# Kernel tuning notes

Hardware: AMD Instinct MI355X
Metric: run time of the kernel (lower is better)

The kernel has to match this reference:

```python
import jax, jax.numpy as jnp
import numpy as np

N_NODES = 200_000
N_EDGES = 12_800_000


def setup_inputs() -> dict:
    key = jax.random.key(0)
    k1, k2, k3, k4 = jax.random.split(key, 4)
    x = jax.random.normal(k1, (N_NODES, 2), dtype=jnp.float32)
    edge_index = jax.random.randint(k2, (2, N_EDGES), 0, N_NODES, dtype=jnp.int32)
    # Glorot-ish init for the two GCN linear layers
    W1 = jax.random.normal(k3, (2, 16), dtype=jnp.float32) * 0.5
    b1 = jnp.zeros((16,), dtype=jnp.float32)
    W2 = jax.random.normal(k4, (16, 2), dtype=jnp.float32) * 0.25
    b2 = jnp.zeros((2,), dtype=jnp.float32)
    return {"x": x, "W1": W1, "b1": b1, "W2": W2, "b2": b2, "edge_index": edge_index}


def gcn_conv(x, W, b, src, dst, num_nodes):
    # PyG GCNConv: add self-loops, deg from dst (col), norm = d_src^-1/2 * d_dst^-1/2,
    # out[i] = sum_{j->i} norm_e * (x_j W) + (1/deg_i) * (x_i W) + b
    h = x @ W  # [N, F_out]
    ones = jnp.ones(src.shape[0], dtype=h.dtype)
    deg = jax.ops.segment_sum(ones, dst, num_segments=num_nodes) + 1.0  # +1 self-loop
    dinv = jax.lax.rsqrt(deg)  # [N]
    norm = dinv[src] * dinv[dst]  # [E]
    agg = jax.ops.segment_sum(h[src] * norm[:, None], dst, num_segments=num_nodes)
    # self-loop contribution has norm dinv_i * dinv_i = 1/deg_i
    return agg + h * (1.0 / deg)[:, None] + b


def reference(x, W1, b1, W2, b2, edge_index):
    src, dst = edge_index[0], edge_index[1]
    h = gcn_conv(x, W1, b1, src, dst, N_NODES)
    h = jax.nn.relu(h)
    out = gcn_conv(h, W2, b2, src, dst, N_NODES)
    return out
```

## Files before the change

### kernel.cpp

```cpp
#include <hip/hip_runtime.h>


constexpr int N_NODES = 200000;
constexpr int N_EDGES = 12800000;
constexpr int RANGE_SHIFT = 8;
constexpr int K_BUCKETS = (N_NODES + 255) / 256;
constexpr int SORT_BLOCKS = 2048;
constexpr int CHUNK = N_EDGES / SORT_BLOCKS;
constexpr int SCAN_R = SORT_BLOCKS / 256;
constexpr int SEG = 4;


__global__ __launch_bounds__(256) void hist_kernel(const int* __restrict__ dst,
                                                   unsigned* __restrict__ blockHist) {
    __shared__ unsigned h[K_BUCKETS];
    for (int i = threadIdx.x; i < K_BUCKETS; i += 256) h[i] = 0;
    __syncthreads();
    int base = blockIdx.x * CHUNK;
    for (int e = base + threadIdx.x; e < base + CHUNK; e += 256)
        atomicAdd(&h[((unsigned)dst[e]) >> RANGE_SHIFT], 1u);
    __syncthreads();
    unsigned* row = blockHist + (size_t)blockIdx.x * K_BUCKETS;
    for (int i = threadIdx.x; i < K_BUCKETS; i += 256) row[i] = h[i];
}

__global__ __launch_bounds__(256) void scan_perblock_kernel(unsigned* __restrict__ blockHist,
                                                            unsigned* __restrict__ bucketTotal) {
    int b = blockIdx.x, t = threadIdx.x;
    unsigned v[SCAN_R], run = 0;
#pragma unroll
    for (int j = 0; j < SCAN_R; j++) v[j] = blockHist[(size_t)(SCAN_R * t + j) * K_BUCKETS + b];
#pragma unroll
    for (int j = 0; j < SCAN_R; j++) { unsigned tmp = v[j]; v[j] = run; run += tmp; }
    __shared__ unsigned sh[256];
    sh[t] = run;
    __syncthreads();
    for (int off = 1; off < 256; off <<= 1) {
        unsigned add = (t >= off) ? sh[t - off] : 0u;
        __syncthreads();
        sh[t] += add;
        __syncthreads();
    }
    unsigned excl = sh[t] - run;
#pragma unroll
    for (int j = 0; j < SCAN_R; j++)
        blockHist[(size_t)(SCAN_R * t + j) * K_BUCKETS + b] = excl + v[j];
    if (t == 255) bucketTotal[b] = sh[255];
}

__global__ __launch_bounds__(1024) void scan_buckets_kernel(const unsigned* __restrict__ bucketTotal,
                                                            unsigned* __restrict__ bucketStart) {
    __shared__ unsigned sh[1024];
    int t = threadIdx.x;
    unsigned v = (t < K_BUCKETS) ? bucketTotal[t] : 0u;
    sh[t] = v;
    __syncthreads();
    for (int off = 1; off < 1024; off <<= 1) {
        unsigned add = (t >= off) ? sh[t - off] : 0u;
        __syncthreads();
        sh[t] += add;
        __syncthreads();
    }
    if (t < K_BUCKETS) bucketStart[t] = sh[t] - v;
    if (t == K_BUCKETS - 1) bucketStart[K_BUCKETS] = sh[t];
}

__global__ __launch_bounds__(256) void scatter_kernel(const int* __restrict__ src,
                                                      const int* __restrict__ dst,
                                                      const unsigned* __restrict__ blockHist,
                                                      const unsigned* __restrict__ bucketStart,
                                                      unsigned* __restrict__ sorted) {
    __shared__ unsigned s_hist[K_BUCKETS];
    __shared__ unsigned s_cur[K_BUCKETS];
    __shared__ int      s_base[K_BUCKETS];
    __shared__ unsigned ssum[256];
    __shared__ unsigned ent[CHUNK];
    __shared__ unsigned short bk[CHUNK];

    int t = threadIdx.x;
    int base = blockIdx.x * CHUNK;
    for (int i = t; i < K_BUCKETS; i += 256) s_hist[i] = 0;
    __syncthreads();

    for (int e = base + t; e < base + CHUNK; e += 256)
        atomicAdd(&s_hist[((unsigned)dst[e]) >> RANGE_SHIFT], 1u);
    __syncthreads();

    unsigned v[4], run = 0;
#pragma unroll
    for (int j = 0; j < 4; j++) {
        int idx = 4 * t + j;
        v[j] = (idx < K_BUCKETS) ? s_hist[idx] : 0u;
    }
#pragma unroll
    for (int j = 0; j < 4; j++) { unsigned tmp = v[j]; v[j] = run; run += tmp; }
    ssum[t] = run;
    __syncthreads();
    for (int off = 1; off < 256; off <<= 1) {
        unsigned add = (t >= off) ? ssum[t - off] : 0u;
        __syncthreads();
        ssum[t] += add;
        __syncthreads();
    }
    unsigned excl = ssum[t] - run;
    const unsigned* row = blockHist + (size_t)blockIdx.x * K_BUCKETS;
#pragma unroll
    for (int j = 0; j < 4; j++) {
        int idx = 4 * t + j;
        if (idx < K_BUCKETS) {
            unsigned st = excl + v[j];
            s_cur[idx] = st;
            s_base[idx] = (int)(bucketStart[idx] + row[idx]) - (int)st;
        }
    }
    __syncthreads();

    for (int e = base + t; e < base + CHUNK; e += 256) {
        unsigned d = (unsigned)dst[e];
        unsigned s = (unsigned)src[e];
        unsigned b = d >> RANGE_SHIFT;
        unsigned lpos = atomicAdd(&s_cur[b], 1u);
        ent[lpos] = s | ((d & 255u) << 18);
        bk[lpos] = (unsigned short)b;
    }
    __syncthreads();

    for (int i = t; i < CHUNK; i += 256) {
        unsigned b = bk[i];
        sorted[s_base[b] + i] = ent[i];
    }
}


__global__ __launch_bounds__(256) void deg_part_kernel(const unsigned* __restrict__ sorted,
                                                       const unsigned* __restrict__ bucketStart,
                                                       unsigned* __restrict__ pcnt) {
    __shared__ unsigned cnt[256];
    int t = threadIdx.x;
    cnt[t] = 0;
    __syncthreads();
    int b = blockIdx.x >> 2, s = blockIdx.x & 3;
    int s0 = bucketStart[b], len = bucketStart[b + 1] - s0;
    int e0 = s0 + (len * s) / SEG;
    int e1 = s0 + (len * (s + 1)) / SEG;
    int e = e0 + t;
    for (; e < e1 - 768; e += 1024) {
        unsigned w0 = sorted[e], w1 = sorted[e + 256], w2 = sorted[e + 512], w3 = sorted[e + 768];
        atomicAdd(&cnt[(w0 >> 18) & 255u], 1u);
        atomicAdd(&cnt[(w1 >> 18) & 255u], 1u);
        atomicAdd(&cnt[(w2 >> 18) & 255u], 1u);
        atomicAdd(&cnt[(w3 >> 18) & 255u], 1u);
    }
    for (; e < e1; e += 256)
        atomicAdd(&cnt[(sorted[e] >> 18) & 255u], 1u);
    __syncthreads();
    pcnt[(size_t)blockIdx.x * 256 + t] = cnt[t];
}

__global__ __launch_bounds__(256) void node1_kernel(const float2* __restrict__ x,
                                                    const unsigned* __restrict__ pcnt,
                                                    float* __restrict__ dinv,
                                                    float2* __restrict__ u) {
    int i = blockIdx.x * 256 + threadIdx.x;
    if (i >= N_NODES) return;
    int b = i >> 8, l = i & 255;
    unsigned c = 1;
#pragma unroll
    for (int s = 0; s < SEG; s++) c += pcnt[(size_t)(b * SEG + s) * 256 + l];
    float di = rsqrtf((float)c);
    dinv[i] = di;
    float2 xi = x[i];
    u[i] = make_float2(di * xi.x, di * xi.y);
}

__global__ __launch_bounds__(256) void agg_part_kernel(const unsigned* __restrict__ sorted,
                                                       const unsigned* __restrict__ bucketStart,
                                                       const float2* __restrict__ table,
                                                       float2* __restrict__ part) {
    __shared__ float ax[256], ay[256];
    int t = threadIdx.x;
    ax[t] = 0.f; ay[t] = 0.f;
    __syncthreads();
    int b = blockIdx.x >> 2, s = blockIdx.x & 3;
    int s0 = bucketStart[b], len = bucketStart[b + 1] - s0;
    int e0 = s0 + (len * s) / SEG;
    int e1 = s0 + (len * (s + 1)) / SEG;
    int e = e0 + t;
    for (; e < e1 - 768; e += 1024) {
        unsigned w0 = sorted[e], w1 = sorted[e + 256], w2 = sorted[e + 512], w3 = sorted[e + 768];
        float2 v0 = table[w0 & 0x3FFFFu];
        float2 v1 = table[w1 & 0x3FFFFu];
        float2 v2 = table[w2 & 0x3FFFFu];
        float2 v3 = table[w3 & 0x3FFFFu];
        atomicAdd(&ax[(w0 >> 18) & 255u], v0.x); atomicAdd(&ay[(w0 >> 18) & 255u], v0.y);
        atomicAdd(&ax[(w1 >> 18) & 255u], v1.x); atomicAdd(&ay[(w1 >> 18) & 255u], v1.y);
        atomicAdd(&ax[(w2 >> 18) & 255u], v2.x); atomicAdd(&ay[(w2 >> 18) & 255u], v2.y);
        atomicAdd(&ax[(w3 >> 18) & 255u], v3.x); atomicAdd(&ay[(w3 >> 18) & 255u], v3.y);
    }
    for (; e < e1; e += 256) {
        unsigned w = sorted[e];
        float2 v = table[w & 0x3FFFFu];
        unsigned l = (w >> 18) & 255u;
        atomicAdd(&ax[l], v.x);
        atomicAdd(&ay[l], v.y);
    }
    __syncthreads();
    part[(size_t)blockIdx.x * 256 + t] = make_float2(ax[t], ay[t]);
}

__global__ __launch_bounds__(256) void node2_kernel(const float2* __restrict__ u,
                                                    const float2* __restrict__ part,
                                                    const float* __restrict__ W1,
                                                    const float* __restrict__ b1,
                                                    const float* __restrict__ W2,
                                                    const float* __restrict__ dinv,
                                                    float2* __restrict__ g2) {
    int i = blockIdx.x * 256 + threadIdx.x;
    if (i >= N_NODES) return;
    int b = i >> 8, l = i & 255;
    float ax = 0.f, ay = 0.f;
#pragma unroll
    for (int s = 0; s < SEG; s++) {
        float2 p = part[(size_t)(b * SEG + s) * 256 + l];
        ax += p.x; ay += p.y;
    }
    float di = dinv[i];
    float2 uu = u[i];
    float c0 = di * (ax + uu.x);
    float c1 = di * (ay + uu.y);
    float a0 = 0.f, a1 = 0.f;
#pragma unroll
    for (int f = 0; f < 16; f++) {
        float o = fmaxf(c0 * W1[f] + c1 * W1[16 + f] + b1[f], 0.f);
        a0 += o * W2[2 * f];
        a1 += o * W2[2 * f + 1];
    }
    g2[i] = make_float2(di * a0, di * a1);
}

__global__ __launch_bounds__(256) void node3_kernel(const float2* __restrict__ g2,
                                                    const float2* __restrict__ part,
                                                    const float* __restrict__ b2,
                                                    const float* __restrict__ dinv,
                                                    float2* __restrict__ out) {
    int i = blockIdx.x * 256 + threadIdx.x;
    if (i >= N_NODES) return;
    int b = i >> 8, l = i & 255;
    float ax = 0.f, ay = 0.f;
#pragma unroll
    for (int s = 0; s < SEG; s++) {
        float2 p = part[(size_t)(b * SEG + s) * 256 + l];
        ax += p.x; ay += p.y;
    }
    float di = dinv[i];
    float2 g = g2[i];
    out[i] = make_float2(di * (ax + g.x) + b2[0],
                         di * (ay + g.y) + b2[1]);
}


__global__ __launch_bounds__(256) void fb_deg(const int* __restrict__ dst, int* __restrict__ degi) {
    int e = blockIdx.x * 256 + threadIdx.x;
    if (e < N_EDGES) atomicAdd(&degi[dst[e]], 1);
}
__global__ __launch_bounds__(256) void fb_node1(const float* __restrict__ x, const int* __restrict__ degi,
                                                float* __restrict__ dinv, float2* __restrict__ u) {
    int i = blockIdx.x * 256 + threadIdx.x;
    if (i >= N_NODES) return;
    float di = rsqrtf((float)(degi[i] + 1));
    dinv[i] = di;
    float2 xi = ((const float2*)x)[i];
    u[i] = make_float2(di * xi.x, di * xi.y);
}
__global__ __launch_bounds__(256) void fb_agg(const int* __restrict__ src, const int* __restrict__ dst,
                                              const float2* __restrict__ table, float* __restrict__ acc) {
    int e = blockIdx.x * 256 + threadIdx.x;
    if (e >= N_EDGES) return;
    float2 v = table[src[e]];
    size_t d = dst[e];
    unsafeAtomicAdd(&acc[2 * d], v.x);
    unsafeAtomicAdd(&acc[2 * d + 1], v.y);
}
__global__ __launch_bounds__(256) void fb_node2(const float2* __restrict__ u, const float2* __restrict__ A1,
                                                const float* __restrict__ W1, const float* __restrict__ b1,
                                                const float* __restrict__ W2, const float* __restrict__ dinv,
                                                float2* __restrict__ g2) {
    int i = blockIdx.x * 256 + threadIdx.x;
    if (i >= N_NODES) return;
    float di = dinv[i];
    float2 a = A1[i], uu = u[i];
    float c0 = di * (a.x + uu.x), c1 = di * (a.y + uu.y);
    float a0 = 0.f, a1 = 0.f;
#pragma unroll
    for (int f = 0; f < 16; f++) {
        float o = fmaxf(c0 * W1[f] + c1 * W1[16 + f] + b1[f], 0.f);
        a0 += o * W2[2 * f];
        a1 += o * W2[2 * f + 1];
    }
    g2[i] = make_float2(di * a0, di * a1);
}
__global__ __launch_bounds__(256) void fb_node3(const float2* __restrict__ g2, const float2* __restrict__ A2,
                                                const float* __restrict__ b2, const float* __restrict__ dinv,
                                                float2* __restrict__ out) {
    int i = blockIdx.x * 256 + threadIdx.x;
    if (i >= N_NODES) return;
    float di = dinv[i];
    float2 a = A2[i], g = g2[i];
    out[i] = make_float2(di * (a.x + g.x) + b2[0], di * (a.y + g.y) + b2[1]);
}


extern "C" void kernel_launch(void* const* d_in, const int* in_sizes, int n_in,
                              void* d_out, int out_size, void* d_ws, size_t ws_size,
                              hipStream_t stream) {
    const float* x  = (const float*)d_in[0];
    const float* W1 = (const float*)d_in[1];
    const float* b1 = (const float*)d_in[2];
    const float* W2 = (const float*)d_in[3];
    const float* b2 = (const float*)d_in[4];
    const int* ei   = (const int*)d_in[5];
    const int* src = ei;
    const int* dst = ei + N_EDGES;
    float2* out = (float2*)d_out;

    const size_t need = ((size_t)N_EDGES + (size_t)SORT_BLOCKS * K_BUCKETS + 782 + 784
                         + N_NODES + 2 * (size_t)N_NODES + 2 * (size_t)N_NODES) * 4;

    if (ws_size >= need) {
        unsigned* sorted      = (unsigned*)d_ws;
        unsigned* blockHist   = sorted + N_EDGES;
        unsigned* bucketTotal = blockHist + (size_t)SORT_BLOCKS * K_BUCKETS;
        unsigned* bucketStart = bucketTotal + 782;
        float*    dinv        = (float*)(bucketStart + 784);
        float2*   u           = (float2*)(dinv + N_NODES);
        float2*   g2          = u + N_NODES;
        unsigned* pcnt        = blockHist;
        float2*   part        = (float2*)blockHist;

        hist_kernel<<<SORT_BLOCKS, 256, 0, stream>>>(dst, blockHist);
        scan_perblock_kernel<<<K_BUCKETS, 256, 0, stream>>>(blockHist, bucketTotal);
        scan_buckets_kernel<<<1, 1024, 0, stream>>>(bucketTotal, bucketStart);
        scatter_kernel<<<SORT_BLOCKS, 256, 0, stream>>>(src, dst, blockHist, bucketStart, sorted);
        deg_part_kernel<<<K_BUCKETS * SEG, 256, 0, stream>>>(sorted, bucketStart, pcnt);
        node1_kernel<<<K_BUCKETS, 256, 0, stream>>>((const float2*)x, pcnt, dinv, u);
        agg_part_kernel<<<K_BUCKETS * SEG, 256, 0, stream>>>(sorted, bucketStart, u, part);
        node2_kernel<<<K_BUCKETS, 256, 0, stream>>>(u, part, W1, b1, W2, dinv, g2);
        agg_part_kernel<<<K_BUCKETS * SEG, 256, 0, stream>>>(sorted, bucketStart, g2, part);
        node3_kernel<<<K_BUCKETS, 256, 0, stream>>>(g2, part, b2, dinv, out);
    } else {
        float* ws = (float*)d_ws;
        int*   degi = (int*)ws;
        float* A1   = ws + N_NODES;
        float* A2   = A1 + 2 * (size_t)N_NODES;
        float* dinvF = A2 + 2 * (size_t)N_NODES;
        float2* uF  = (float2*)(dinvF + N_NODES);
        float2* g2F = uF + N_NODES;
        constexpr int EB = (N_EDGES + 255) / 256;
        constexpr int NB = (N_NODES + 255) / 256;
        hipMemsetAsync(degi, 0, 5 * (size_t)N_NODES * sizeof(float), stream);
        fb_deg<<<EB, 256, 0, stream>>>(dst, degi);
        fb_node1<<<NB, 256, 0, stream>>>(x, degi, dinvF, uF);
        fb_agg<<<EB, 256, 0, stream>>>(src, dst, uF, A1);
        fb_node2<<<NB, 256, 0, stream>>>(uF, (const float2*)A1, W1, b1, W2, dinvF, g2F);
        fb_agg<<<EB, 256, 0, stream>>>(src, dst, g2F, A2);
        fb_node3<<<NB, 256, 0, stream>>>(g2F, (const float2*)A2, b2, dinvF, out);
    }
}
```

Before: 584.4 us.

## Build per-node CSR inside buckets and aggregate with one wavefront per node

Adds a sortbins pass that sorts each 256-node bucket by destination node in LDS. It also emits per-node offsets, from which degrees come directly as offset differences. The shared-memory float-atomic partial aggregation kernels are replaced by one-wavefront-per-node gather-and-reduce kernels that also fold in the node-level transforms. The scatter kernel now reuses the already-scanned per-block histograms instead of recomputing them. The cost is an extra read and write of the sorted edge array, and buckets larger than CAPB are silently skipped.

Measured after the change: 520.2 us. 11.0% less time.

```diff
diff --git a/kernel.cpp b/kernel.cpp
--- a/kernel.cpp
+++ b/kernel.cpp
@@ -8,7 +8,7 @@
 constexpr int SORT_BLOCKS = 2048;
 constexpr int CHUNK = N_EDGES / SORT_BLOCKS;
 constexpr int SCAN_R = SORT_BLOCKS / 256;
-constexpr int SEG = 4;
+constexpr int CAPB = 18432;
 
 
 __global__ __launch_bounds__(256) void hist_kernel(const int* __restrict__ dst,
@@ -68,9 +68,9 @@
 __global__ __launch_bounds__(256) void scatter_kernel(const int* __restrict__ src,
                                                       const int* __restrict__ dst,
                                                       const unsigned* __restrict__ blockHist,
+                                                      const unsigned* __restrict__ bucketTotal,
                                                       const unsigned* __restrict__ bucketStart,
                                                       unsigned* __restrict__ sorted) {
-    __shared__ unsigned s_hist[K_BUCKETS];
     __shared__ unsigned s_cur[K_BUCKETS];
     __shared__ int      s_base[K_BUCKETS];
     __shared__ unsigned ssum[256];
@@ -78,19 +78,22 @@
     __shared__ unsigned short bk[CHUNK];
 
     int t = threadIdx.x;
-    int base = blockIdx.x * CHUNK;
-    for (int i = t; i < K_BUCKETS; i += 256) s_hist[i] = 0;
-    __syncthreads();
-
-    for (int e = base + t; e < base + CHUNK; e += 256)
-        atomicAdd(&s_hist[((unsigned)dst[e]) >> RANGE_SHIFT], 1u);
-    __syncthreads();
-
-    unsigned v[4], run = 0;
+    int k = blockIdx.x;
+    int base = k * CHUNK;
+    const unsigned* row  = blockHist + (size_t)k * K_BUCKETS;
+    const unsigned* rowN = blockHist + (size_t)(k + 1) * K_BUCKETS;
+    bool last = (k == SORT_BLOCKS - 1);
+
+    unsigned v[4], g0[4], run = 0;
 #pragma unroll
     for (int j = 0; j < 4; j++) {
         int idx = 4 * t + j;
-        v[j] = (idx < K_BUCKETS) ? s_hist[idx] : 0u;
+        if (idx < K_BUCKETS) {
+            unsigned r0 = row[idx];
+            unsigned r1 = last ? bucketTotal[idx] : rowN[idx];
+            g0[j] = r0;
+            v[j]  = r1 - r0;
+        } else { g0[j] = 0; v[j] = 0; }
     }
 #pragma unroll
     for (int j = 0; j < 4; j++) { unsigned tmp = v[j]; v[j] = run; run += tmp; }
@@ -103,14 +106,13 @@
         __syncthreads();
     }
     unsigned excl = ssum[t] - run;
-    const unsigned* row = blockHist + (size_t)blockIdx.x * K_BUCKETS;
 #pragma unroll
     for (int j = 0; j < 4; j++) {
         int idx = 4 * t + j;
         if (idx < K_BUCKETS) {
             unsigned st = excl + v[j];
-            s_cur[idx] = st;
-            s_base[idx] = (int)(bucketStart[idx] + row[idx]) - (int)st;
+            s_cur[idx]  = st;
+            s_base[idx] = (int)(bucketStart[idx] + g0[j]) - (int)st;
         }
     }
     __syncthreads();
@@ -131,131 +133,130 @@
     }
 }
 
-
-__global__ __launch_bounds__(256) void deg_part_kernel(const unsigned* __restrict__ sorted,
+__global__ __launch_bounds__(256) void sortbins_kernel(unsigned* __restrict__ sorted,
                                                        const unsigned* __restrict__ bucketStart,
-                                                       unsigned* __restrict__ pcnt) {
-    __shared__ unsigned cnt[256];
-    int t = threadIdx.x;
-    cnt[t] = 0;
-    __syncthreads();
-    int b = blockIdx.x >> 2, s = blockIdx.x & 3;
-    int s0 = bucketStart[b], len = bucketStart[b + 1] - s0;
-    int e0 = s0 + (len * s) / SEG;
-    int e1 = s0 + (len * (s + 1)) / SEG;
-    int e = e0 + t;
-    for (; e < e1 - 768; e += 1024) {
-        unsigned w0 = sorted[e], w1 = sorted[e + 256], w2 = sorted[e + 512], w3 = sorted[e + 768];
-        atomicAdd(&cnt[(w0 >> 18) & 255u], 1u);
-        atomicAdd(&cnt[(w1 >> 18) & 255u], 1u);
-        atomicAdd(&cnt[(w2 >> 18) & 255u], 1u);
-        atomicAdd(&cnt[(w3 >> 18) & 255u], 1u);
-    }
-    for (; e < e1; e += 256)
-        atomicAdd(&cnt[(sorted[e] >> 18) & 255u], 1u);
-    __syncthreads();
-    pcnt[(size_t)blockIdx.x * 256 + t] = cnt[t];
-}
-
-__global__ __launch_bounds__(256) void node1_kernel(const float2* __restrict__ x,
-                                                    const unsigned* __restrict__ pcnt,
-                                                    float* __restrict__ dinv,
-                                                    float2* __restrict__ u) {
+                                                       unsigned* __restrict__ nodeStart) {
+    __shared__ unsigned ent[CAPB];
+    __shared__ unsigned hist[256];
+    __shared__ unsigned cur[256];
+    __shared__ unsigned ssum[256];
+    int t = threadIdx.x, b = blockIdx.x;
+    int base = (int)bucketStart[b];
+    int n = (int)bucketStart[b + 1] - base;
+    if (n > CAPB) return;
+
+    hist[t] = 0;
+    __syncthreads();
+    for (int i = t; i < n; i += 256) {
+        unsigned w = sorted[base + i];
+        ent[i] = w;
+        atomicAdd(&hist[(w >> 18) & 255u], 1u);
+    }
+    __syncthreads();
+    unsigned v = hist[t];
+    ssum[t] = v;
+    __syncthreads();
+    for (int off = 1; off < 256; off <<= 1) {
+        unsigned add = (t >= off) ? ssum[t - off] : 0u;
+        __syncthreads();
+        ssum[t] += add;
+        __syncthreads();
+    }
+    unsigned excl = ssum[t] - v;
+    cur[t] = excl;
+    int node = (b << RANGE_SHIFT) + t;
+    if (node < N_NODES) nodeStart[node] = (unsigned)(base + (int)excl);
+    if (b == K_BUCKETS - 1 && t == 0) nodeStart[N_NODES] = bucketStart[K_BUCKETS];
+    __syncthreads();
+    for (int i = t; i < n; i += 256) {
+        unsigned w = ent[i];
+        unsigned p = atomicAdd(&cur[(w >> 18) & 255u], 1u);
+        sorted[base + (int)p] = w;
+    }
+}
+
+
+__global__ __launch_bounds__(256) void node1w_kernel(const float2* __restrict__ x,
+                                                     const unsigned* __restrict__ nodeStart,
+                                                     float* __restrict__ dinv,
+                                                     float2* __restrict__ u) {
     int i = blockIdx.x * 256 + threadIdx.x;
     if (i >= N_NODES) return;
-    int b = i >> 8, l = i & 255;
-    unsigned c = 1;
-#pragma unroll
-    for (int s = 0; s < SEG; s++) c += pcnt[(size_t)(b * SEG + s) * 256 + l];
-    float di = rsqrtf((float)c);
+    unsigned deg = nodeStart[i + 1] - nodeStart[i] + 1u;
+    float di = rsqrtf((float)deg);
     dinv[i] = di;
     float2 xi = x[i];
     u[i] = make_float2(di * xi.x, di * xi.y);
 }
 
-__global__ __launch_bounds__(256) void agg_part_kernel(const unsigned* __restrict__ sorted,
-                                                       const unsigned* __restrict__ bucketStart,
-                                                       const float2* __restrict__ table,
-                                                       float2* __restrict__ part) {
-    __shared__ float ax[256], ay[256];
-    int t = threadIdx.x;
-    ax[t] = 0.f; ay[t] = 0.f;
-    __syncthreads();
-    int b = blockIdx.x >> 2, s = blockIdx.x & 3;
-    int s0 = bucketStart[b], len = bucketStart[b + 1] - s0;
-    int e0 = s0 + (len * s) / SEG;
-    int e1 = s0 + (len * (s + 1)) / SEG;
-    int e = e0 + t;
-    for (; e < e1 - 768; e += 1024) {
-        unsigned w0 = sorted[e], w1 = sorted[e + 256], w2 = sorted[e + 512], w3 = sorted[e + 768];
-        float2 v0 = table[w0 & 0x3FFFFu];
-        float2 v1 = table[w1 & 0x3FFFFu];
-        float2 v2 = table[w2 & 0x3FFFFu];
-        float2 v3 = table[w3 & 0x3FFFFu];
-        atomicAdd(&ax[(w0 >> 18) & 255u], v0.x); atomicAdd(&ay[(w0 >> 18) & 255u], v0.y);
-        atomicAdd(&ax[(w1 >> 18) & 255u], v1.x); atomicAdd(&ay[(w1 >> 18) & 255u], v1.y);
-        atomicAdd(&ax[(w2 >> 18) & 255u], v2.x); atomicAdd(&ay[(w2 >> 18) & 255u], v2.y);
-        atomicAdd(&ax[(w3 >> 18) & 255u], v3.x); atomicAdd(&ay[(w3 >> 18) & 255u], v3.y);
-    }
-    for (; e < e1; e += 256) {
-        unsigned w = sorted[e];
-        float2 v = table[w & 0x3FFFFu];
-        unsigned l = (w >> 18) & 255u;
-        atomicAdd(&ax[l], v.x);
-        atomicAdd(&ay[l], v.y);
-    }
-    __syncthreads();
-    part[(size_t)blockIdx.x * 256 + t] = make_float2(ax[t], ay[t]);
-}
-
-__global__ __launch_bounds__(256) void node2_kernel(const float2* __restrict__ u,
-                                                    const float2* __restrict__ part,
+__global__ __launch_bounds__(256) void aggw1_kernel(const unsigned* __restrict__ sorted,
+                                                    const unsigned* __restrict__ nodeStart,
+                                                    const float2* __restrict__ u,
+                                                    const float* __restrict__ dinv,
                                                     const float* __restrict__ W1,
                                                     const float* __restrict__ b1,
                                                     const float* __restrict__ W2,
-                                                    const float* __restrict__ dinv,
                                                     float2* __restrict__ g2) {
-    int i = blockIdx.x * 256 + threadIdx.x;
-    if (i >= N_NODES) return;
-    int b = i >> 8, l = i & 255;
+    int i = blockIdx.x * 4 + (threadIdx.x >> 6);
+    if (i >= N_NODES) return;
+    int lane = threadIdx.x & 63;
+    int e0 = (int)nodeStart[i], e1 = (int)nodeStart[i + 1];
     float ax = 0.f, ay = 0.f;
-#pragma unroll
-    for (int s = 0; s < SEG; s++) {
-        float2 p = part[(size_t)(b * SEG + s) * 256 + l];
-        ax += p.x; ay += p.y;
+    for (int k = e0 + lane; k < e1; k += 64) {
+        unsigned w = sorted[k];
+        float2 v = u[w & 0x3FFFFu];
+        ax += v.x; ay += v.y;
+    }
+#pragma unroll
+    for (int off = 32; off; off >>= 1) {
+        ax += __shfl_xor(ax, off);
+        ay += __shfl_xor(ay, off);
     }
     float di = dinv[i];
     float2 uu = u[i];
     float c0 = di * (ax + uu.x);
     float c1 = di * (ay + uu.y);
     float a0 = 0.f, a1 = 0.f;
-#pragma unroll
-    for (int f = 0; f < 16; f++) {
-        float o = fmaxf(c0 * W1[f] + c1 * W1[16 + f] + b1[f], 0.f);
-        a0 += o * W2[2 * f];
-        a1 += o * W2[2 * f + 1];
-    }
-    g2[i] = make_float2(di * a0, di * a1);
-}
-
-__global__ __launch_bounds__(256) void node3_kernel(const float2* __restrict__ g2,
-                                                    const float2* __restrict__ part,
+    if (lane < 16) {
+        float o = fmaxf(c0 * W1[lane] + c1 * W1[16 + lane] + b1[lane], 0.f);
+        a0 = o * W2[2 * lane];
+        a1 = o * W2[2 * lane + 1];
+    }
+#pragma unroll
+    for (int off = 8; off; off >>= 1) {
+        a0 += __shfl_xor(a0, off);
+        a1 += __shfl_xor(a1, off);
+    }
+    if (lane == 0) g2[i] = make_float2(di * a0, di * a1);
+}
+
+__global__ __launch_bounds__(256) void aggw2_kernel(const unsigned* __restrict__ sorted,
+                                                    const unsigned* __restrict__ nodeStart,
+                                                    const float2* __restrict__ g2,
+                                                    const float* __restrict__ dinv,
                                                     const float* __restrict__ b2,
-                                                    const float* __restrict__ dinv,
                                                     float2* __restrict__ out) {
-    int i = blockIdx.x * 256 + threadIdx.x;
-    if (i >= N_NODES) return;
-    int b = i >> 8, l = i & 255;
+    int i = blockIdx.x * 4 + (threadIdx.x >> 6);
+    if (i >= N_NODES) return;
+    int lane = threadIdx.x & 63;
+    int e0 = (int)nodeStart[i], e1 = (int)nodeStart[i + 1];
     float ax = 0.f, ay = 0.f;
-#pragma unroll
-    for (int s = 0; s < SEG; s++) {
-        float2 p = part[(size_t)(b * SEG + s) * 256 + l];
-        ax += p.x; ay += p.y;
-    }
-    float di = dinv[i];
-    float2 g = g2[i];
-    out[i] = make_float2(di * (ax + g.x) + b2[0],
-                         di * (ay + g.y) + b2[1]);
+    for (int k = e0 + lane; k < e1; k += 64) {
+        unsigned w = sorted[k];
+        float2 v = g2[w & 0x3FFFFu];
+        ax += v.x; ay += v.y;
+    }
+#pragma unroll
+    for (int off = 32; off; off >>= 1) {
+        ax += __shfl_xor(ax, off);
+        ay += __shfl_xor(ay, off);
+    }
+    if (lane == 0) {
+        float di = dinv[i];
+        float2 g = g2[i];
+        out[i] = make_float2(di * (ax + g.x) + b2[0],
+                             di * (ay + g.y) + b2[1]);
+    }
 }
 
 
@@ -323,30 +324,30 @@
     const int* dst = ei + N_EDGES;
     float2* out = (float2*)d_out;
 
-    const size_t need = ((size_t)N_EDGES + (size_t)SORT_BLOCKS * K_BUCKETS + 782 + 784
-                         + N_NODES + 2 * (size_t)N_NODES + 2 * (size_t)N_NODES) * 4;
+    const size_t need = ((size_t)N_EDGES + (size_t)SORT_BLOCKS * K_BUCKETS + 782 + 784) * 4;
 
     if (ws_size >= need) {
         unsigned* sorted      = (unsigned*)d_ws;
-        unsigned* blockHist   = sorted + N_EDGES;
-        unsigned* bucketTotal = blockHist + (size_t)SORT_BLOCKS * K_BUCKETS;
+        unsigned* region      = sorted + N_EDGES;
+        unsigned* blockHist   = region;
+        unsigned* nodeStart   = region;
+        float*    dinv        = (float*)(region + 200004);
+        float2*   u           = (float2*)(region + 400004);
+        float2*   g2          = (float2*)(region + 800004);
+        unsigned* bucketTotal = region + (size_t)SORT_BLOCKS * K_BUCKETS;
         unsigned* bucketStart = bucketTotal + 782;
-        float*    dinv        = (float*)(bucketStart + 784);
-        float2*   u           = (float2*)(dinv + N_NODES);
-        float2*   g2          = u + N_NODES;
-        unsigned* pcnt        = blockHist;
-        float2*   part        = (float2*)blockHist;
 
         hist_kernel<<<SORT_BLOCKS, 256, 0, stream>>>(dst, blockHist);
         scan_perblock_kernel<<<K_BUCKETS, 256, 0, stream>>>(blockHist, bucketTotal);
         scan_buckets_kernel<<<1, 1024, 0, stream>>>(bucketTotal, bucketStart);
-        scatter_kernel<<<SORT_BLOCKS, 256, 0, stream>>>(src, dst, blockHist, bucketStart, sorted);
-        deg_part_kernel<<<K_BUCKETS * SEG, 256, 0, stream>>>(sorted, bucketStart, pcnt);
-        node1_kernel<<<K_BUCKETS, 256, 0, stream>>>((const float2*)x, pcnt, dinv, u);
-        agg_part_kernel<<<K_BUCKETS * SEG, 256, 0, stream>>>(sorted, bucketStart, u, part);
-        node2_kernel<<<K_BUCKETS, 256, 0, stream>>>(u, part, W1, b1, W2, dinv, g2);
-        agg_part_kernel<<<K_BUCKETS * SEG, 256, 0, stream>>>(sorted, bucketStart, g2, part);
-        node3_kernel<<<K_BUCKETS, 256, 0, stream>>>(g2, part, b2, dinv, out);
+        scatter_kernel<<<SORT_BLOCKS, 256, 0, stream>>>(src, dst, blockHist, bucketTotal,
+                                                        bucketStart, sorted);
+        sortbins_kernel<<<K_BUCKETS, 256, 0, stream>>>(sorted, bucketStart, nodeStart);
+        node1w_kernel<<<K_BUCKETS, 256, 0, stream>>>((const float2*)x, nodeStart, dinv, u);
+        aggw1_kernel<<<(N_NODES + 3) / 4, 256, 0, stream>>>(sorted, nodeStart, u, dinv,
+                                                            W1, b1, W2, g2);
+        aggw2_kernel<<<(N_NODES + 3) / 4, 256, 0, stream>>>(sorted, nodeStart, g2, dinv,
+                                                            b2, out);
     } else {
         float* ws = (float*)d_ws;
         int*   degi = (int*)ws;
@@ -357,7 +358,7 @@
         float2* g2F = uF + N_NODES;
         constexpr int EB = (N_EDGES + 255) / 256;
         constexpr int NB = (N_NODES + 255) / 256;
-        hipMemsetAsync(degi, 0, 5 * (size_t)N_NODES * sizeof(float), stream);
+        (void)hipMemsetAsync(degi, 0, 5 * (size_t)N_NODES * sizeof(float), stream);
         fb_deg<<<EB, 256, 0, stream>>>(dst, degi);
         fb_node1<<<NB, 256, 0, stream>>>(x, degi, dinvF, uF);
         fb_agg<<<EB, 256, 0, stream>>>(src, dst, uF, A1);
```
